# Performance work log

Hardware: AMD Instinct MI355X
Metric: run time of the kernel (lower is better)

## Reference

```python
import jax, jax.numpy as jnp
import numpy as np
import math

D_MODEL = 512
H = 8
DK = D_MODEL // H  # 64
B, S = 2, 4096


def setup_inputs() -> dict:
    key = jax.random.key(0)
    ks = jax.random.split(key, 11)
    sc = 1.0 / math.sqrt(D_MODEL)
    return {
        "query": jax.random.normal(ks[0], (B, S, D_MODEL), jnp.float32),
        "key": jax.random.normal(ks[1], (B, S, D_MODEL), jnp.float32),
        "value": jax.random.normal(ks[2], (B, S, D_MODEL), jnp.float32),
        "Wq": jax.random.normal(ks[3], (D_MODEL, D_MODEL), jnp.float32) * sc,
        "bq": jnp.zeros((D_MODEL,), jnp.float32),
        "Wk": jax.random.normal(ks[4], (D_MODEL, D_MODEL), jnp.float32) * sc,
        "bk": jnp.zeros((D_MODEL,), jnp.float32),
        "Wv": jax.random.normal(ks[5], (D_MODEL, D_MODEL), jnp.float32) * sc,
        "bv": jnp.zeros((D_MODEL,), jnp.float32),
        "Wo": jax.random.normal(ks[6], (D_MODEL, D_MODEL), jnp.float32) * sc,
        "bo": jnp.zeros((D_MODEL,), jnp.float32),
    }


def reference(query, key, value, Wq, bq, Wk, bk, Wv, bv, Wo, bo):
    b = query.shape[0]
    # projections; W stored [in, out]
    def proj(x, W, bias):
        y = x @ W + bias                      # [B,S,h*dk]
        return y.reshape(b, -1, H, DK).transpose(0, 2, 1, 3)  # [B,h,S,dk]

    q = proj(query, Wq, bq)
    k = proj(key, Wk, bk)
    v = proj(value, Wv, bv)
    scores = jnp.einsum("bhqd,bhkd->bhqk", q, k) / math.sqrt(DK)
    attn = jax.nn.softmax(scores, axis=-1)    # [B,h,Sq,Sk]
    ctx = jnp.einsum("bhqk,bhkd->bhqd", attn, v)
    ctx = ctx.transpose(0, 2, 1, 3).reshape(b, -1, H * DK)  # [B,S,d_model]
    return ctx @ Wo + bo
```

## Files before the change

### kernel.cpp

```cpp
#include <hip/hip_runtime.h>
#include <hip/hip_bf16.h>

#define DM   512
#define HEADS 8
#define DKH  64
#define BATCH 2
#define SEQ  4096

typedef float  f32x4  __attribute__((ext_vector_type(4)));
typedef float  f32x16 __attribute__((ext_vector_type(16)));
typedef __bf16 bf16x8 __attribute__((ext_vector_type(8)));
typedef __bf16 bf16x2 __attribute__((ext_vector_type(2)));

static __device__ __forceinline__ f32x4 mfma16(bf16x8 a, bf16x8 b, f32x4 c) {
    return __builtin_amdgcn_mfma_f32_16x16x32_bf16(a, b, c, 0, 0, 0);
}
static __device__ __forceinline__ f32x16 mfma32(bf16x8 a, bf16x8 b, f32x16 c) {
    return __builtin_amdgcn_mfma_f32_32x32x16_bf16(a, b, c, 0, 0, 0);
}

#define GLD16(gp, lp) __builtin_amdgcn_global_load_lds( \
    (const __attribute__((address_space(1))) void*)(gp), \
    (__attribute__((address_space(3))) void*)(lp), 16, 0, 0)

#define WAITVM(n) asm volatile("s_waitcnt vmcnt(" #n ")" ::: "memory")

static __device__ __forceinline__ void barrier_sync() {
    __builtin_amdgcn_sched_barrier(0);
    asm volatile("" ::: "memory");
    __builtin_amdgcn_s_barrier();
    asm volatile("" ::: "memory");
    __builtin_amdgcn_sched_barrier(0);
}

struct Cvt3 { const float* s[3]; __bf16* d[3]; };

__global__ __launch_bounds__(256) void convert_x3(Cvt3 a) {
    const float* s = a.s[blockIdx.y];
    __bf16* d = a.d[blockIdx.y];
    const size_t i = ((size_t)blockIdx.x * 256 + threadIdx.x) * 8;
    f32x4 f0 = *(const f32x4*)&s[i];
    f32x4 f1 = *(const f32x4*)&s[i + 4];
    bf16x8 v;
    v[0] = (__bf16)f0[0]; v[1] = (__bf16)f0[1]; v[2] = (__bf16)f0[2]; v[3] = (__bf16)f0[3];
    v[4] = (__bf16)f1[0]; v[5] = (__bf16)f1[1]; v[6] = (__bf16)f1[2]; v[7] = (__bf16)f1[3];
    *(bf16x8*)&d[i] = v;
}

struct WtAll { const float* W[4]; __bf16* Wt[4]; };

__global__ __launch_bounds__(256) void wt_convert_all(WtAll a) {
    const float* W = a.W[blockIdx.z];
    __bf16* Wt = a.Wt[blockIdx.z];
    __shared__ float tile[32][33];
    const int tx = threadIdx.x & 31, ty = threadIdx.x >> 5;
    const int nb = blockIdx.x * 32, kb = blockIdx.y * 32;
#pragma unroll
    for (int i = 0; i < 4; ++i)
        tile[ty + 8 * i][tx] = W[(size_t)(kb + ty + 8 * i) * DM + nb + tx];
    __syncthreads();
#pragma unroll
    for (int i = 0; i < 4; ++i)
        Wt[(size_t)(nb + ty + 8 * i) * DM + kb + tx] = (__bf16)tile[tx][ty + 8 * i];
}

struct Ptr3 { const __bf16* A; const __bf16* Bt; const float* bias; void* Out; float ascale; };
struct GemmArgs { Ptr3 p[3]; };

template <bool OUT_BF16, int BN>
__global__ __launch_bounds__(256) void gemm_tile(GemmArgs args) {
    constexpr int BGLD = BN / 32;
    constexpr int NJ   = BN / 32;
    constexpr int NT   = DM / 64;
    __shared__ __bf16 Al[2][128][64];
    __shared__ __bf16 Bl[2][BN][64];
    const Ptr3 P = args.p[blockIdx.z];
    const int tid = threadIdx.x;
    const int lane = tid & 63, wid = tid >> 6;
    const int lq = lane & 15, hi = lane >> 4;
    const int m0 = blockIdx.x * 128, n0 = blockIdx.y * BN;
    const int wm = (wid >> 1) * 64, wn = (wid & 1) * (BN / 2);

    const int lrow = lane >> 3, lslot = lane & 7;
    const __bf16* gaP[4];
#pragma unroll
    for (int i = 0; i < 4; ++i) {
        const int r = wid * 32 + i * 8 + lrow;
        const int s = lslot ^ ((r ^ (r >> 3)) & 7);
        gaP[i] = P.A + (size_t)(m0 + r) * DM + s * 8;
    }
    const __bf16* gbP[BGLD];
#pragma unroll
    for (int i = 0; i < BGLD; ++i) {
        const int r = wid * (BN / 4) + i * 8 + lrow;
        const int s = lslot ^ ((r ^ (r >> 3)) & 7);
        gbP[i] = P.Bt + (size_t)(n0 + r) * DM + s * 8;
    }
    auto stage = [&](int kt, int buf) {
        const int k0 = kt * 64;
#pragma unroll
        for (int i = 0; i < 4; ++i)
            GLD16(gaP[i] + k0, &Al[buf][wid * 32 + i * 8][0]);
#pragma unroll
        for (int i = 0; i < BGLD; ++i)
            GLD16(gbP[i] + k0, &Bl[buf][wid * (BN / 4) + i * 8][0]);
    };

    int baseA[4], swA[4];
#pragma unroll
    for (int i = 0; i < 4; ++i) {
        const int r = wm + i * 16 + lq;
        baseA[i] = r * 128;
        swA[i] = (((r ^ (r >> 3)) & 7) << 4);
    }
    int baseB[NJ], swB[NJ];
#pragma unroll
    for (int j = 0; j < NJ; ++j) {
        const int r = wn + j * 16 + lq;
        baseB[j] = r * 128;
        swB[j] = (((r ^ (r >> 3)) & 7) << 4);
    }

    f32x4 acc[4][NJ] = {};

    stage(0, 0);
    stage(1, 1);
    for (int kt = 0; kt < NT; ++kt) {
        const int cur = kt & 1;
        if (kt + 1 < NT) {
            if (BN == 128) { WAITVM(8); } else { WAITVM(6); }
        } else { WAITVM(0); }
        barrier_sync();
        const char* Ab = (const char*)&Al[cur][0][0];
        const char* Bb = (const char*)&Bl[cur][0][0];
        __builtin_amdgcn_s_setprio(1);
#pragma unroll
        for (int ks = 0; ks < 2; ++ks) {
            const int off = ks * 64 + hi * 16;
            bf16x8 af[4], bfv[NJ];
#pragma unroll
            for (int i = 0; i < 4; ++i)
                af[i] = *(const bf16x8*)(Ab + baseA[i] + (off ^ swA[i]));
#pragma unroll
            for (int j = 0; j < NJ; ++j)
                bfv[j] = *(const bf16x8*)(Bb + baseB[j] + (off ^ swB[j]));
#pragma unroll
            for (int i = 0; i < 4; ++i)
#pragma unroll
                for (int j = 0; j < NJ; ++j)
                    acc[i][j] = mfma16(af[i], bfv[j], acc[i][j]);
        }
        __builtin_amdgcn_s_setprio(0);
        if (kt + 2 < NT) {
            barrier_sync();
            stage(kt + 2, cur);
        }
    }

    const float* bias = P.bias;
    const float asc = P.ascale;
#pragma unroll
    for (int j = 0; j < NJ; ++j) {
        const int n = n0 + wn + j * 16 + lq;
        const float bv = bias[n];
#pragma unroll
        for (int i = 0; i < 4; ++i) {
#pragma unroll
            for (int r = 0; r < 4; ++r) {
                const int m = m0 + wm + i * 16 + hi * 4 + r;
                const float v = (acc[i][j][r] + bv) * asc;
                if (OUT_BF16) ((__bf16*)P.Out)[(size_t)m * DM + n] = (__bf16)v;
                else          ((float*)P.Out)[(size_t)m * DM + n] = v;
            }
        }
    }
}

__global__ __launch_bounds__(256) void v_transpose(const __bf16* __restrict__ Vp,
                                                   __bf16* __restrict__ Vt) {
    __shared__ __bf16 tile[64][72];
    const int tid = threadIdx.x;
    const int tt = blockIdx.x * 64;
    const int bh = blockIdx.y, b = bh >> 3, h = bh & 7;
#pragma unroll
    for (int i = 0; i < 2; ++i) {
        int c = tid + 256 * i, row = c >> 3, cc = c & 7;
        *(bf16x8*)&tile[row][cc * 8] =
            *(const bf16x8*)&Vp[(size_t)(b * SEQ + tt + row) * DM + h * DKH + cc * 8];
    }
    __syncthreads();
#pragma unroll
    for (int i = 0; i < 2; ++i) {
        int c = tid + 256 * i, row = c >> 3, cc = c & 7;
        bf16x8 v;
#pragma unroll
        for (int j = 0; j < 8; ++j) v[j] = tile[cc * 8 + j][row];
        *(bf16x8*)&Vt[(size_t)(bh * DKH + row) * SEQ + tt + cc * 8] = v;
    }
}

template <bool SPLIT>
__global__ __launch_bounds__(256, 4) void flash_attn4(const __bf16* __restrict__ Qp,
                                                      const __bf16* __restrict__ Kp,
                                                      const __bf16* __restrict__ Vt,
                                                      __bf16* __restrict__ O0,
                                                      __bf16* __restrict__ O1,
                                                      float* __restrict__ MLM,
                                                      float* __restrict__ MLL) {
    __shared__ __bf16 Kl[2][64][64];
    __shared__ __bf16 Vl[2][64][64];
    __shared__ float  Lbuf[4][32];

    const int tid = threadIdx.x, lane = tid & 63, w = tid >> 6;
    const int c = lane & 31, h = lane >> 5;
    const int bh = blockIdx.y, b = bh >> 3, hd = bh & 7;
    const int qbase = blockIdx.x * 128 + w * 32;
    const int kvoff = SPLIT ? blockIdx.z * (SEQ / 2) : 0;
    const int NT = SPLIT ? (SEQ / 2) / 64 : SEQ / 64;

    bf16x8 qf[4];
#pragma unroll
    for (int t = 0; t < 4; ++t)
        qf[t] = *(const bf16x8*)&Qp[(size_t)(b * SEQ + qbase + c) * DM + hd * DKH + 16 * t + 8 * h];

    const int r0 = w * 16 + (lane >> 3);
    const int r1 = r0 + 8;
    const int s0 = (lane & 7) ^ ((r0 ^ (r0 >> 3)) & 7);
    const int s1 = (lane & 7) ^ ((r1 ^ (r1 >> 3)) & 7);
    const __bf16* kg0 = Kp + (size_t)(b * SEQ + kvoff + r0) * DM + hd * DKH + s0 * 8;
    const __bf16* kg1 = Kp + (size_t)(b * SEQ + kvoff + r1) * DM + hd * DKH + s1 * 8;
    const __bf16* vg0 = Vt + (size_t)(bh * DKH + r0) * SEQ + kvoff + s0 * 8;
    const __bf16* vg1 = Vt + (size_t)(bh * DKH + r1) * SEQ + kvoff + s1 * 8;

    const int swz0 = (c ^ (c >> 3)) & 7;
    const int swz1 = ((32 + c) ^ ((32 + c) >> 3)) & 7;
    const int rowb0 = c * 128, rowb1 = (32 + c) * 128;
    const char* kb = (const char*)&Kl[0][0][0];
    const char* vb = (const char*)&Vl[0][0][0];

    auto stage = [&](int t, int buf) {
        const size_t ko = (size_t)t * 64 * DM, vo = (size_t)t * 64;
        GLD16(kg0 + ko, &Kl[buf][w * 16][0]);
        GLD16(kg1 + ko, &Kl[buf][w * 16 + 8][0]);
        GLD16(vg0 + vo, &Vl[buf][w * 16][0]);
        GLD16(vg1 + vo, &Vl[buf][w * 16 + 8][0]);
    };

    bf16x8 vone;
#pragma unroll
    for (int j = 0; j < 8; ++j) vone[j] = (__bf16)1.0f;

    f32x16 acc0 = {}, acc1 = {}, lacc = {};
    float m_run = -__builtin_inff();

    stage(0, 0);
    stage(1, 1);

    for (int t = 0; t < NT; ++t) {
        const int cur = t & 1;
        if (t + 1 < NT) { WAITVM(4); } else { WAITVM(0); }
        barrier_sync();
        const char* kc = kb + cur * 8192;
        const char* vc = vb + cur * 8192;

        f32x16 sa = {}, sb = {};
        __builtin_amdgcn_s_setprio(1);
#pragma unroll
        for (int tt = 0; tt < 4; ++tt) {
            bf16x8 kf0 = *(const bf16x8*)(kc + rowb0 + (((2 * tt + h) ^ swz0) << 4));
            sa = mfma32(kf0, qf[tt], sa);
            bf16x8 kf1 = *(const bf16x8*)(kc + rowb1 + (((2 * tt + h) ^ swz1) << 4));
            sb = mfma32(kf1, qf[tt], sb);
        }
        __builtin_amdgcn_s_setprio(0);

        float mx = fmaxf(sa[0], sa[1]);
#pragma unroll
        for (int r = 2; r < 16; r += 2) mx = fmaxf(mx, fmaxf(sa[r], sa[r + 1]));
#pragma unroll
        for (int r = 0; r < 16; r += 2) mx = fmaxf(mx, fmaxf(sb[r], sb[r + 1]));
        mx = fmaxf(mx, __shfl_xor(mx, 32));
        if (!__all(mx <= m_run + 8.f)) {
            const float mnew = fmaxf(m_run, mx);
            const float al = __builtin_amdgcn_exp2f(m_run - mnew);
            m_run = mnew;
            if (lane < 32) Lbuf[w][lane] = al;
#pragma unroll
            for (int r = 0; r < 16; ++r) {
                const float a2 = Lbuf[w][(r & 3) + 8 * (r >> 2) + 4 * h];
                acc0[r] *= a2; acc1[r] *= a2; lacc[r] *= a2;
            }
        }

        int ua[4][2], ub[4][2];
#pragma unroll
        for (int q4 = 0; q4 < 4; ++q4) {
            float p0 = __builtin_amdgcn_exp2f(sa[4 * q4 + 0] - m_run);
            float p1 = __builtin_amdgcn_exp2f(sa[4 * q4 + 1] - m_run);
            float p2 = __builtin_amdgcn_exp2f(sa[4 * q4 + 2] - m_run);
            float p3 = __builtin_amdgcn_exp2f(sa[4 * q4 + 3] - m_run);
            bf16x2 t0; t0[0] = (__bf16)p0; t0[1] = (__bf16)p1;
            bf16x2 t1; t1[0] = (__bf16)p2; t1[1] = (__bf16)p3;
            ua[q4][0] = __builtin_bit_cast(int, t0);
            ua[q4][1] = __builtin_bit_cast(int, t1);
        }
#pragma unroll
        for (int q4 = 0; q4 < 4; ++q4) {
            float p0 = __builtin_amdgcn_exp2f(sb[4 * q4 + 0] - m_run);
            float p1 = __builtin_amdgcn_exp2f(sb[4 * q4 + 1] - m_run);
            float p2 = __builtin_amdgcn_exp2f(sb[4 * q4 + 2] - m_run);
            float p3 = __builtin_amdgcn_exp2f(sb[4 * q4 + 3] - m_run);
            bf16x2 t0; t0[0] = (__bf16)p0; t0[1] = (__bf16)p1;
            bf16x2 t1; t1[0] = (__bf16)p2; t1[1] = (__bf16)p3;
            ub[q4][0] = __builtin_bit_cast(int, t0);
            ub[q4][1] = __builtin_bit_cast(int, t1);
        }

#pragma unroll
        for (int tg = 0; tg < 4; ++tg) {
            int x0, y0, x1, y1;
            if (tg < 2) {
                x0 = ua[2 * tg][0]; y0 = ua[2 * tg + 1][0];
                x1 = ua[2 * tg][1]; y1 = ua[2 * tg + 1][1];
            } else {
                x0 = ub[2 * (tg - 2)][0]; y0 = ub[2 * (tg - 2) + 1][0];
                x1 = ub[2 * (tg - 2)][1]; y1 = ub[2 * (tg - 2) + 1][1];
            }
            asm("v_permlane32_swap_b32 %0, %1" : "+v"(x0), "+v"(y0));
            asm("v_permlane32_swap_b32 %0, %1" : "+v"(x1), "+v"(y1));
            union { int i4[4]; bf16x8 v; } pf;
            pf.i4[0] = x0; pf.i4[1] = x1; pf.i4[2] = y0; pf.i4[3] = y1;
            bf16x8 vf0 = *(const bf16x8*)(vc + rowb0 + (((2 * tg + h) ^ swz0) << 4));
            bf16x8 vf1 = *(const bf16x8*)(vc + rowb1 + (((2 * tg + h) ^ swz1) << 4));
            __builtin_amdgcn_s_setprio(1);
            acc0 = mfma32(pf.v, vf0, acc0);
            acc1 = mfma32(pf.v, vf1, acc1);
            lacc = mfma32(pf.v, vone, lacc);
            __builtin_amdgcn_s_setprio(0);
        }

        if (t + 2 < NT) {
            barrier_sync();
            stage(t + 2, cur);
        }
    }

    if (SPLIT) {
        __bf16* pp = blockIdx.z ? O1 : O0;
#pragma unroll
        for (int r = 0; r < 16; ++r) {
            const int qr = (r & 3) + 8 * (r >> 2) + 4 * h;
            const size_t off = (size_t)(b * SEQ + qbase + qr) * DM + hd * DKH;
            pp[off + c]      = (__bf16)acc0[r];
            pp[off + 32 + c] = (__bf16)acc1[r];
        }
        const int zo = blockIdx.z * 16 + bh;
        if (h == 0) MLM[(size_t)zo * SEQ + qbase + c] = m_run;
        if (c == 0) {
#pragma unroll
            for (int r = 0; r < 16; ++r) {
                const int qr = (r & 3) + 8 * (r >> 2) + 4 * h;
                MLL[(size_t)zo * SEQ + qbase + qr] = lacc[r];
            }
        }
    } else {
        __bf16* outp = O0 + (size_t)(b * SEQ + qbase) * DM + hd * DKH;
#pragma unroll
        for (int r = 0; r < 16; ++r) {
            const int qr = (r & 3) + 8 * (r >> 2) + 4 * h;
            const float li = 1.f / lacc[r];
            outp[(size_t)qr * DM + c]      = (__bf16)(acc0[r] * li);
            outp[(size_t)qr * DM + 32 + c] = (__bf16)(acc1[r] * li);
        }
    }
}

__global__ __launch_bounds__(256) void combine(const __bf16* __restrict__ P0,
                                               const __bf16* __restrict__ P1,
                                               const float* __restrict__ MLM,
                                               const float* __restrict__ MLL,
                                               __bf16* __restrict__ Ctx) {
    const int row = blockIdx.x;
    const int b = row >> 12, q = row & (SEQ - 1);
    const int col = threadIdx.x * 2;
    const int head = col >> 6;
    const int bh = b * HEADS + head;
    const float m0 = MLM[(size_t)bh * SEQ + q];
    const float m1 = MLM[(size_t)(16 + bh) * SEQ + q];
    const float l0 = MLL[(size_t)bh * SEQ + q];
    const float l1 = MLL[(size_t)(16 + bh) * SEQ + q];
    const float m = fmaxf(m0, m1);
    const float e0 = __builtin_amdgcn_exp2f(m0 - m);
    const float e1 = __builtin_amdgcn_exp2f(m1 - m);
    const float inv = 1.f / (l0 * e0 + l1 * e1);
    const float f0 = e0 * inv, f1 = e1 * inv;
    const size_t idx = (size_t)row * DM + col;
    bf16x2 a = *(const bf16x2*)&P0[idx];
    bf16x2 bb = *(const bf16x2*)&P1[idx];
    bf16x2 o;
    o[0] = (__bf16)((float)a[0] * f0 + (float)bb[0] * f1);
    o[1] = (__bf16)((float)a[1] * f0 + (float)bb[1] * f1);
    *(bf16x2*)&Ctx[idx] = o;
}

extern "C" void kernel_launch(void* const* d_in, const int* in_sizes, int n_in,
                              void* d_out, int out_size, void* d_ws, size_t ws_size,
                              hipStream_t stream) {
    (void)in_sizes; (void)n_in; (void)out_size;
    const float* query = (const float*)d_in[0];
    const float* key_  = (const float*)d_in[1];
    const float* value = (const float*)d_in[2];
    const float* Wq = (const float*)d_in[3];
    const float* bq = (const float*)d_in[4];
    const float* Wk = (const float*)d_in[5];
    const float* bk = (const float*)d_in[6];
    const float* Wv = (const float*)d_in[7];
    const float* bv = (const float*)d_in[8];
    const float* Wo = (const float*)d_in[9];
    const float* bo = (const float*)d_in[10];

    char* ws = (char*)d_ws;
    const size_t WSZ = (size_t)512 * 1024;
    const size_t XSZ = (size_t)8 * 1024 * 1024;
    const float QSC = 0.125f * 1.4426950408889634f;
    if (ws_size < 4 * WSZ + 7 * XSZ) return;

    __bf16* Wtq = (__bf16*)(ws);
    __bf16* Wtk = (__bf16*)(ws + WSZ);
    __bf16* Wtv = (__bf16*)(ws + 2 * WSZ);
    __bf16* Wto = (__bf16*)(ws + 3 * WSZ);
    char* xb = ws + 4 * WSZ;
    __bf16* Qb = (__bf16*)(xb);
    __bf16* Kb = (__bf16*)(xb + XSZ);
    __bf16* Vb = (__bf16*)(xb + 2 * XSZ);
    __bf16* Qp = (__bf16*)(xb + 3 * XSZ);
    __bf16* Kp = (__bf16*)(xb + 4 * XSZ);
    __bf16* Vp = (__bf16*)(xb + 5 * XSZ);
    __bf16* Vt = (__bf16*)(xb + 6 * XSZ);
    __bf16* Ctx = Vp;
    __bf16* P0 = Qb;
    __bf16* P1 = Kb;
    float* MLM = (float*)Vb;
    float* MLL = MLM + 2 * 16 * SEQ;

    Cvt3 cv;
    cv.s[0] = query; cv.s[1] = key_; cv.s[2] = value;
    cv.d[0] = Qb; cv.d[1] = Kb; cv.d[2] = Vb;
    convert_x3<<<dim3(2048, 3), 256, 0, stream>>>(cv);

    WtAll wa;
    wa.W[0] = Wq; wa.W[1] = Wk; wa.W[2] = Wv; wa.W[3] = Wo;
    wa.Wt[0] = Wtq; wa.Wt[1] = Wtk; wa.Wt[2] = Wtv; wa.Wt[3] = Wto;
    wt_convert_all<<<dim3(16, 16, 4), 256, 0, stream>>>(wa);

    GemmArgs qa;
    qa.p[0] = {Qb, Wtq, bq, Qp, QSC};
    qa.p[1] = {Kb, Wtk, bk, Kp, 1.0f};
    qa.p[2] = {Vb, Wtv, bv, Vp, 1.0f};
    gemm_tile<true, 128><<<dim3(64, 4, 3), 256, 0, stream>>>(qa);

    v_transpose<<<dim3(SEQ / 64, BATCH * HEADS), 256, 0, stream>>>(Vp, Vt);

    flash_attn4<true><<<dim3(SEQ / 128, BATCH * HEADS, 2), 256, 0, stream>>>(
        Qp, Kp, Vt, P0, P1, MLM, MLL);

    combine<<<dim3(BATCH * SEQ), 256, 0, stream>>>(P0, P1, MLM, MLL, Ctx);

    GemmArgs oa;
    oa.p[0] = {Ctx, Wto, bo, d_out, 1.0f};
    oa.p[1] = oa.p[0]; oa.p[2] = oa.p[0];
    gemm_tile<false, 64><<<dim3(64, 8, 1), 256, 0, stream>>>(oa);
}
```

Measured before the change: 266.9 us.

## Fuse V transpose into projection epilogue and remap attention block order

The V projection GEMM now writes its output directly in the transposed per-head layout, so the separate v_transpose kernel and its extra read/write pass are removed. The flash attention kernel remaps its block index so consecutive blocks are spread across XCDs, aiming to improve L2 locality for K/V sharing. Its pipeline also changes from depth-2 prefetch with vmcnt waits to a simpler single-ahead prefetch with full __syncthreads each iteration. The simpler sync may expose more load latency, and the transposed epilogue writes are strided 8-byte stores.

```diff
diff --git a/kernel.cpp b/kernel.cpp
--- a/kernel.cpp
+++ b/kernel.cpp
@@ -10,6 +10,7 @@
 typedef float  f32x4  __attribute__((ext_vector_type(4)));
 typedef float  f32x16 __attribute__((ext_vector_type(16)));
 typedef __bf16 bf16x8 __attribute__((ext_vector_type(8)));
+typedef __bf16 bf16x4 __attribute__((ext_vector_type(4)));
 typedef __bf16 bf16x2 __attribute__((ext_vector_type(2)));
 
 static __device__ __forceinline__ f32x4 mfma16(bf16x8 a, bf16x8 b, f32x4 c) {
@@ -64,7 +65,7 @@
         Wt[(size_t)(nb + ty + 8 * i) * DM + kb + tx] = (__bf16)tile[tx][ty + 8 * i];
 }
 
-struct Ptr3 { const __bf16* A; const __bf16* Bt; const float* bias; void* Out; float ascale; };
+struct Ptr3 { const __bf16* A; const __bf16* Bt; const float* bias; void* Out; float ascale; int vt; };
 struct GemmArgs { Ptr3 p[3]; };
 
 template <bool OUT_BF16, int BN>
@@ -159,48 +160,43 @@
 
     const float* bias = P.bias;
     const float asc = P.ascale;
-#pragma unroll
-    for (int j = 0; j < NJ; ++j) {
-        const int n = n0 + wn + j * 16 + lq;
-        const float bv = bias[n];
-#pragma unroll
-        for (int i = 0; i < 4; ++i) {
-#pragma unroll
-            for (int r = 0; r < 4; ++r) {
-                const int m = m0 + wm + i * 16 + hi * 4 + r;
-                const float v = (acc[i][j][r] + bv) * asc;
-                if (OUT_BF16) ((__bf16*)P.Out)[(size_t)m * DM + n] = (__bf16)v;
-                else          ((float*)P.Out)[(size_t)m * DM + n] = v;
+    if (OUT_BF16 && P.vt) {
+#pragma unroll
+        for (int j = 0; j < NJ; ++j) {
+            const int n = n0 + wn + j * 16 + lq;
+            const int head = n >> 6, dk = n & 63;
+            const float bv = bias[n];
+#pragma unroll
+            for (int i = 0; i < 4; ++i) {
+                const int m = m0 + wm + i * 16 + hi * 4;
+                const int b = m >> 12, q = m & (SEQ - 1);
+                bf16x4 vv;
+#pragma unroll
+                for (int r = 0; r < 4; ++r) vv[r] = (__bf16)((acc[i][j][r] + bv) * asc);
+                *(bf16x4*)&((__bf16*)P.Out)[((size_t)((b * HEADS + head) * DKH + dk)) * SEQ + q] = vv;
             }
         }
-    }
-}
-
-__global__ __launch_bounds__(256) void v_transpose(const __bf16* __restrict__ Vp,
-                                                   __bf16* __restrict__ Vt) {
-    __shared__ __bf16 tile[64][72];
-    const int tid = threadIdx.x;
-    const int tt = blockIdx.x * 64;
-    const int bh = blockIdx.y, b = bh >> 3, h = bh & 7;
-#pragma unroll
-    for (int i = 0; i < 2; ++i) {
-        int c = tid + 256 * i, row = c >> 3, cc = c & 7;
-        *(bf16x8*)&tile[row][cc * 8] =
-            *(const bf16x8*)&Vp[(size_t)(b * SEQ + tt + row) * DM + h * DKH + cc * 8];
-    }
-    __syncthreads();
-#pragma unroll
-    for (int i = 0; i < 2; ++i) {
-        int c = tid + 256 * i, row = c >> 3, cc = c & 7;
-        bf16x8 v;
-#pragma unroll
-        for (int j = 0; j < 8; ++j) v[j] = tile[cc * 8 + j][row];
-        *(bf16x8*)&Vt[(size_t)(bh * DKH + row) * SEQ + tt + cc * 8] = v;
+    } else {
+#pragma unroll
+        for (int j = 0; j < NJ; ++j) {
+            const int n = n0 + wn + j * 16 + lq;
+            const float bv = bias[n];
+#pragma unroll
+            for (int i = 0; i < 4; ++i) {
+#pragma unroll
+                for (int r = 0; r < 4; ++r) {
+                    const int m = m0 + wm + i * 16 + hi * 4 + r;
+                    const float v = (acc[i][j][r] + bv) * asc;
+                    if (OUT_BF16) ((__bf16*)P.Out)[(size_t)m * DM + n] = (__bf16)v;
+                    else          ((float*)P.Out)[(size_t)m * DM + n] = v;
+                }
+            }
+        }
     }
 }
 
 template <bool SPLIT>
-__global__ __launch_bounds__(256, 4) void flash_attn4(const __bf16* __restrict__ Qp,
+__global__ __launch_bounds__(256, 4) void flash_attn5(const __bf16* __restrict__ Qp,
                                                       const __bf16* __restrict__ Kp,
                                                       const __bf16* __restrict__ Vt,
                                                       __bf16* __restrict__ O0,
@@ -213,9 +209,18 @@
 
     const int tid = threadIdx.x, lane = tid & 63, w = tid >> 6;
     const int c = lane & 31, h = lane >> 5;
-    const int bh = blockIdx.y, b = bh >> 3, hd = bh & 7;
-    const int qbase = blockIdx.x * 128 + w * 32;
-    const int kvoff = SPLIT ? blockIdx.z * (SEQ / 2) : 0;
+
+    constexpr int NBLK = 32 * 16 * (SPLIT ? 2 : 1);
+    constexpr int CPX = NBLK / 8;
+    int fid = blockIdx.x + 32 * (blockIdx.y + 16 * blockIdx.z);
+    fid = (fid & 7) * CPX + (fid >> 3);
+    const int qt = fid & 31;
+    const int bh = (fid >> 5) & 15;
+    const int zz = SPLIT ? (fid >> 9) : 0;
+
+    const int b = bh >> 3, hd = bh & 7;
+    const int qbase = qt * 128 + w * 32;
+    const int kvoff = SPLIT ? zz * (SEQ / 2) : 0;
     const int NT = SPLIT ? (SEQ / 2) / 64 : SEQ / 64;
 
     bf16x8 qf[4];
@@ -254,12 +259,11 @@
     float m_run = -__builtin_inff();
 
     stage(0, 0);
-    stage(1, 1);
+    __syncthreads();
 
     for (int t = 0; t < NT; ++t) {
         const int cur = t & 1;
-        if (t + 1 < NT) { WAITVM(4); } else { WAITVM(0); }
-        barrier_sync();
+        if (t + 1 < NT) stage(t + 1, cur ^ 1);
         const char* kc = kb + cur * 8192;
         const char* vc = vb + cur * 8192;
 
@@ -338,15 +342,11 @@
             lacc = mfma32(pf.v, vone, lacc);
             __builtin_amdgcn_s_setprio(0);
         }
-
-        if (t + 2 < NT) {
-            barrier_sync();
-            stage(t + 2, cur);
-        }
+        __syncthreads();
     }
 
     if (SPLIT) {
-        __bf16* pp = blockIdx.z ? O1 : O0;
+        __bf16* pp = zz ? O1 : O0;
 #pragma unroll
         for (int r = 0; r < 16; ++r) {
             const int qr = (r & 3) + 8 * (r >> 2) + 4 * h;
@@ -354,7 +354,7 @@
             pp[off + c]      = (__bf16)acc0[r];
             pp[off + 32 + c] = (__bf16)acc1[r];
         }
-        const int zo = blockIdx.z * 16 + bh;
+        const int zo = zz * 16 + bh;
         if (h == 0) MLM[(size_t)zo * SEQ + qbase + c] = m_run;
         if (c == 0) {
 #pragma unroll
@@ -435,9 +435,8 @@
     __bf16* Vb = (__bf16*)(xb + 2 * XSZ);
     __bf16* Qp = (__bf16*)(xb + 3 * XSZ);
     __bf16* Kp = (__bf16*)(xb + 4 * XSZ);
-    __bf16* Vp = (__bf16*)(xb + 5 * XSZ);
-    __bf16* Vt = (__bf16*)(xb + 6 * XSZ);
-    __bf16* Ctx = Vp;
+    __bf16* Vt = (__bf16*)(xb + 5 * XSZ);
+    __bf16* Ctx = (__bf16*)(xb + 6 * XSZ);
     __bf16* P0 = Qb;
     __bf16* P1 = Kb;
     float* MLM = (float*)Vb;
@@ -454,20 +453,18 @@
     wt_convert_all<<<dim3(16, 16, 4), 256, 0, stream>>>(wa);
 
     GemmArgs qa;
-    qa.p[0] = {Qb, Wtq, bq, Qp, QSC};
-    qa.p[1] = {Kb, Wtk, bk, Kp, 1.0f};
-    qa.p[2] = {Vb, Wtv, bv, Vp, 1.0f};
+    qa.p[0] = {Qb, Wtq, bq, Qp, QSC, 0};
+    qa.p[1] = {Kb, Wtk, bk, Kp, 1.0f, 0};
+    qa.p[2] = {Vb, Wtv, bv, Vt, 1.0f, 1};
     gemm_tile<true, 128><<<dim3(64, 4, 3), 256, 0, stream>>>(qa);
 
-    v_transpose<<<dim3(SEQ / 64, BATCH * HEADS), 256, 0, stream>>>(Vp, Vt);
-
-    flash_attn4<true><<<dim3(SEQ / 128, BATCH * HEADS, 2), 256, 0, stream>>>(
+    flash_attn5<true><<<dim3(SEQ / 128, BATCH * HEADS, 2), 256, 0, stream>>>(
         Qp, Kp, Vt, P0, P1, MLM, MLL);
 
     combine<<<dim3(BATCH * SEQ), 256, 0, stream>>>(P0, P1, MLM, MLL, Ctx);
 
     GemmArgs oa;
-    oa.p[0] = {Ctx, Wto, bo, d_out, 1.0f};
+    oa.p[0] = {Ctx, Wto, bo, d_out, 1.0f, 0};
     oa.p[1] = oa.p[0]; oa.p[2] = oa.p[0];
     gemm_tile<false, 64><<<dim3(64, 8, 1), 256, 0, stream>>>(oa);
 }
```

Result: faster. 256.0 us (-4.1%).
